# Kernel tuning notes

Measured on AMD Instinct MI355X. Metric: run time of the kernel, lower is better.

## Reference

```python
import jax, jax.numpy as jnp
import numpy as np

KSZ = 5   # local window size per spatial dim
NH = 4    # num_channels -> attention heads
EPS = 1e-6

def rmsnorm(x, w):
    return x * jax.lax.rsqrt(jnp.mean(x * x, axis=-1, keepdims=True) + EPS) * w

def local_windows(x, ksz):
    # x: [B, D, H, W, C] -> [B, D, H, W, ksz**3, C] zero-padded SAME windows
    B, D, H, Wd, C = x.shape
    xt = jnp.transpose(x, (0, 4, 1, 2, 3))  # NCDHW
    p = jax.lax.conv_general_dilated_patches(xt, (ksz, ksz, ksz), (1, 1, 1), 'SAME')
    p = p.reshape(B, C, ksz ** 3, D, H, Wd)  # channel-major patch layout
    return jnp.transpose(p, (0, 3, 4, 5, 2, 1))

def forward(x, norm1_w, attn_norm_w, norm2_w, wq, wk, wv, wo, gate_w, up_w, down_w):
    B, D, H, Wd, C = x.shape
    hd = C // NH
    k3 = KSZ ** 3
    h = rmsnorm(x, norm1_w)
    q = (h @ wq).reshape(B, D, H, Wd, NH, hd)
    k = h @ wk
    v = h @ wv
    kwin = local_windows(k, KSZ).reshape(B, D, H, Wd, k3, NH, hd)
    vwin = local_windows(v, KSZ).reshape(B, D, H, Wd, k3, NH, hd)
    scores = jnp.einsum('bxyzhe,bxyzkhe->bxyzhk', q, kwin) / jnp.sqrt(jnp.float32(hd))
    ones = jnp.ones((1, D, H, Wd, 1), x.dtype)
    valid = local_windows(ones, KSZ)[..., 0] > 0.5  # [1,D,H,W,k3] padding mask
    scores = jnp.where(valid[:, :, :, :, None, :], scores, jnp.float32(-1e9))
    attn = jax.nn.softmax(scores, axis=-1)
    o = jnp.einsum('bxyzhk,bxyzkhe->bxyzhe', attn, vwin).reshape(B, D, H, Wd, C)
    x = x + rmsnorm(o @ wo, attn_norm_w)
    h2 = rmsnorm(x, norm2_w)
    x = x + (jax.nn.silu(h2 @ gate_w) * (h2 @ up_w)) @ down_w  # SwiGLU (dropout=eval)
    return x

def setup_inputs():
    key = jax.random.key(0)
    ks = jax.random.split(key, 8)
    width, hidden = 128, 512
    s = 0.02
    return {
        'x': jax.random.normal(ks[0], (1, 16, 16, 16, width), jnp.float32),
        'norm1_w': jnp.ones((width,), jnp.float32),
        'attn_norm_w': jnp.ones((width,), jnp.float32),
        'norm2_w': jnp.ones((width,), jnp.float32),
        'wq': jax.random.normal(ks[1], (width, width), jnp.float32) * s,
        'wk': jax.random.normal(ks[2], (width, width), jnp.float32) * s,
        'wv': jax.random.normal(ks[3], (width, width), jnp.float32) * s,
        'wo': jax.random.normal(ks[4], (width, width), jnp.float32) * s,
        'gate_w': jax.random.normal(ks[5], (width, hidden), jnp.float32) * s,
        'up_w': jax.random.normal(ks[6], (width, hidden), jnp.float32) * s,
        'down_w': jax.random.normal(ks[7], (hidden, width), jnp.float32) * s,
    }

def reference(x, norm1_w, attn_norm_w, norm2_w, wq, wk, wv, wo, gate_w, up_w, down_w):
    return forward(x, norm1_w, attn_norm_w, norm2_w, wq, wk, wv, wo, gate_w, up_w, down_w)
```

## Files before the change

kernel.cpp:

```cpp
#include <hip/hip_runtime.h>
#include <hip/hip_bf16.h>

#define NVOX 4096
#define C    128
#define HID  512
#define EPSF 1e-6f

typedef __attribute__((ext_vector_type(8))) short bf16x8;
typedef __attribute__((ext_vector_type(4))) float f32x4;

__device__ __forceinline__ short f2bs(float f) {
    __hip_bfloat16 h = __float2bfloat16(f);
    short s; __builtin_memcpy(&s, &h, 2); return s;
}
__device__ __forceinline__ float bs2f(unsigned short u) {
    return __uint_as_float(((unsigned)u) << 16);
}

__device__ __forceinline__ bf16x8 lda(const short* hs, int lane, int ks) {
    int r = lane & 15, g = lane >> 4;
    int col = (ks * 32 + g * 8) ^ ((r & 7) << 3);
    return *(const bf16x8*)(hs + r * 128 + col);
}

__device__ __forceinline__ float wave_rsum(float s) {
    s += __shfl_xor(s, 32); s += __shfl_xor(s, 16); s += __shfl_xor(s, 8);
    s += __shfl_xor(s, 4);  s += __shfl_xor(s, 2);  s += __shfl_xor(s, 1);
    return s;
}

__global__ __launch_bounds__(512) void k_prep(
    const float* __restrict__ wq, const float* __restrict__ wk,
    const float* __restrict__ wv, const float* __restrict__ wo,
    const float* __restrict__ gw, const float* __restrict__ uw,
    const float* __restrict__ dw, short* __restrict__ wsw)
{
    int id = blockIdx.x * 512 + threadIdx.x;
    const float* src; int base, ct, ks, lane, N, KS;
    if (id < 8192) {
        int m = id >> 11, loc = id & 2047;
        src = (m == 0) ? wq : (m == 1) ? wk : (m == 2) ? wv : wo;
        base = m << 14; N = 128; KS = 4;
        ct = loc >> 8; ks = (loc >> 6) & 3; lane = loc & 63;
    } else if (id < 16384) {
        int loc = id - 8192;
        src = gw; base = 65536; N = 512; KS = 4;
        ct = loc >> 8; ks = (loc >> 6) & 3; lane = loc & 63;
    } else if (id < 24576) {
        int loc = id - 16384;
        src = uw; base = 131072; N = 512; KS = 4;
        ct = loc >> 8; ks = (loc >> 6) & 3; lane = loc & 63;
    } else {
        int loc = id - 24576;
        src = dw; base = 196608; N = 128; KS = 16;
        ct = loc >> 10; ks = (loc >> 6) & 15; lane = loc & 63;
    }
    int k0 = ks * 32 + (lane >> 4) * 8;
    int c  = ct * 16 + (lane & 15);
    bf16x8 v;
    #pragma unroll
    for (int j = 0; j < 8; j++) v[j] = f2bs(src[(size_t)(k0 + j) * N + c]);
    *(bf16x8*)(wsw + base + (((ct * KS + ks) * 64 + lane) << 3)) = v;
}

__global__ __launch_bounds__(256) void k_qkv(
    const float* __restrict__ x, const float* __restrict__ n1,
    const short* __restrict__ wsw,
    short* __restrict__ qbf, short* __restrict__ kbf, short* __restrict__ vbf)
{
    __shared__ short hs[2048];
    const int r0 = blockIdx.x * 16, t = threadIdx.x;
    const int w = t >> 6, lane = t & 63;

    #pragma unroll
    for (int i = 0; i < 4; i++) {
        int r = w * 4 + i;
        const float* xp = x + (size_t)(r0 + r) * 128;
        float v0 = xp[lane], v1 = xp[lane + 64];
        float s = wave_rsum(fmaf(v0, v0, v1 * v1));
        float sc = rsqrtf(s * (1.0f / 128.0f) + EPSF);
        int p3 = (r & 7) << 3;
        hs[r * 128 + (lane ^ p3)]        = f2bs(v0 * sc * n1[lane]);
        hs[r * 128 + ((lane + 64) ^ p3)] = f2bs(v1 * sc * n1[lane + 64]);
    }
    __syncthreads();

    bf16x8 af[4];
    #pragma unroll
    for (int ks = 0; ks < 4; ks++) af[ks] = lda(hs, lane, ks);

    const int rb = (lane >> 4) * 4, cl = lane & 15, cb = w * 32;
    #pragma unroll
    for (int m = 0; m < 3; m++) {
        const short* wb = wsw + (m << 14);
        f32x4 a0 = {0.f,0.f,0.f,0.f}, a1 = {0.f,0.f,0.f,0.f};
        #pragma unroll
        for (int ks = 0; ks < 4; ks++) {
            bf16x8 b0 = *(const bf16x8*)(wb + ((((w * 2) * 4 + ks) * 64 + lane) << 3));
            bf16x8 b1 = *(const bf16x8*)(wb + ((((w * 2 + 1) * 4 + ks) * 64 + lane) << 3));
            a0 = __builtin_amdgcn_mfma_f32_16x16x32_bf16(af[ks], b0, a0, 0, 0, 0);
            a1 = __builtin_amdgcn_mfma_f32_16x16x32_bf16(af[ks], b1, a1, 0, 0, 0);
        }
        short* outp = (m == 0) ? qbf : (m == 1) ? kbf : vbf;
        #pragma unroll
        for (int i = 0; i < 4; i++) {
            outp[(size_t)(r0 + rb + i) * 128 + cb + cl]      = f2bs(a0[i]);
            outp[(size_t)(r0 + rb + i) * 128 + cb + 16 + cl] = f2bs(a1[i]);
        }
    }
}

__global__ __launch_bounds__(256) void k_attn(
    const short* __restrict__ qbf, const short* __restrict__ kbf,
    const short* __restrict__ vbf, short* __restrict__ obf)
{
    __shared__ __align__(16) char smem[64128];
    short* K_lds = (short*)smem;
    short* PA    = (short*)smem;
    short* S_lds = (short*)(smem + 30720);
    short* VB    = (short*)(smem + 30720);
    short* Q_lds = (short*)(smem + 61440);
    float* inv   = (float*)(smem + 64000);

    const int b = blockIdx.x, head = blockIdx.y, t = threadIdx.x;
    const int ow = (b & 3) * 4, oh = ((b >> 2) & 3) * 4, od = (b >> 4) * 2;
    const int w = t >> 6, lane = t & 63;
    const int g = lane >> 4, r = lane & 15;

    uint4 v0[4] = {}, v1[4] = {};
    {
        int row = t;
        int lw = row & 7, lh = (row >> 3) & 7, ld = row >> 6;
        int gd = od - 2 + ld, gh = oh - 2 + lh, gw_ = ow - 2 + lw;
        int sv = (((unsigned)gd < 16u) && ((unsigned)gh < 16u) && ((unsigned)gw_ < 16u));
        size_t off = ((size_t)(((gd << 4) | gh) << 4 | gw_)) * 128 + head * 32;
        uint4 kc[4];
        #pragma unroll
        for (int c2 = 0; c2 < 4; c2++) {
            kc[c2] = sv ? *(const uint4*)(kbf + off + c2 * 8) : (uint4){0,0,0,0};
            v0[c2] = sv ? *(const uint4*)(vbf + off + c2 * 8) : (uint4){0,0,0,0};
        }
        #pragma unroll
        for (int c2 = 0; c2 < 4; c2++) *(uint4*)&K_lds[row * 40 + c2 * 8] = kc[c2];

        if (t < 128) {
            int row1 = t + 256;
            int lw1 = row1 & 7, lh1 = (row1 >> 3) & 7, ld1 = row1 >> 6;
            int gd1 = od - 2 + ld1, gh1 = oh - 2 + lh1, gw1 = ow - 2 + lw1;
            int sv1 = (((unsigned)gd1 < 16u) && ((unsigned)gh1 < 16u) && ((unsigned)gw1 < 16u));
            size_t off1 = ((size_t)(((gd1 << 4) | gh1) << 4 | gw1)) * 128 + head * 32;
            uint4 kd[4];
            #pragma unroll
            for (int c2 = 0; c2 < 4; c2++) {
                kd[c2] = sv1 ? *(const uint4*)(kbf + off1 + c2 * 8) : (uint4){0,0,0,0};
                v1[c2] = sv1 ? *(const uint4*)(vbf + off1 + c2 * 8) : (uint4){0,0,0,0};
            }
            #pragma unroll
            for (int c2 = 0; c2 < 4; c2++) *(uint4*)&K_lds[row1 * 40 + c2 * 8] = kd[c2];

            int q = t >> 2, c2q = t & 3;
            int gq = ((od + (q >> 4)) << 8) | ((oh + ((q >> 2) & 3)) << 4) | (ow + (q & 3));
            *(uint4*)&Q_lds[q * 40 + c2q * 8] =
                *(const uint4*)(qbf + (size_t)gq * 128 + head * 32 + c2q * 8);
        }
    }
    __syncthreads();

    {
        bf16x8 bq0 = *(const bf16x8*)(Q_lds + r * 40 + g * 8);
        bf16x8 bq1 = *(const bf16x8*)(Q_lds + (16 + r) * 40 + g * 8);
        #pragma unroll
        for (int jj = 0; jj < 6; jj++) {
            int mt = w + jj * 4;
            bf16x8 ak = *(const bf16x8*)(K_lds + (mt * 16 + r) * 40 + g * 8);
            f32x4 a0 = {0.f,0.f,0.f,0.f}, a1 = {0.f,0.f,0.f,0.f};
            a0 = __builtin_amdgcn_mfma_f32_16x16x32_bf16(ak, bq0, a0, 0, 0, 0);
            a1 = __builtin_amdgcn_mfma_f32_16x16x32_bf16(ak, bq1, a1, 0, 0, 0);
            #pragma unroll
            for (int i = 0; i < 4; i++) {
                int key = mt * 16 + g * 4 + i;
                S_lds[key * 40 + r]      = f2bs(a0[i]);
                S_lds[key * 40 + 16 + r] = f2bs(a1[i]);
            }
        }
    }
    __syncthreads();

    {
        const int q = t >> 3, kl = t & 7;
        const int qw_ = q & 3, qh_ = (q >> 2) & 3, qd_ = q >> 4;
        const float isq = 0.17677669529663687f;
        float mx = -1e30f;
        #pragma unroll
        for (int j = 0; j < 48; j++) {
            int k = kl + (j << 3);
            int lw = k & 7, lh = (k >> 3) & 7, ld = k >> 6;
            int ok = ((unsigned)(ld - qd_) <= 4u) & ((unsigned)(lh - qh_) <= 4u)
                   & ((unsigned)(lw - qw_) <= 4u)
                   & ((unsigned)(od - 2 + ld) < 16u) & ((unsigned)(oh - 2 + lh) < 16u)
                   & ((unsigned)(ow - 2 + lw) < 16u);
            float s = bs2f((unsigned short)S_lds[k * 40 + q]) * isq;
            mx = ok ? fmaxf(mx, s) : mx;
        }
        mx = fmaxf(mx, __shfl_xor(mx, 1));
        mx = fmaxf(mx, __shfl_xor(mx, 2));
        mx = fmaxf(mx, __shfl_xor(mx, 4));
        float ssum = 0.f;
        const int pabase = (q >> 4) * 12 * 512 + (q & 15) * 8 + kl;
        #pragma unroll
        for (int j = 0; j < 48; j++) {
            int k = kl + (j << 3);
            int lw = k & 7, lh = (k >> 3) & 7, ld = k >> 6;
            int ok = ((unsigned)(ld - qd_) <= 4u) & ((unsigned)(lh - qh_) <= 4u)
                   & ((unsigned)(lw - qw_) <= 4u)
                   & ((unsigned)(od - 2 + ld) < 16u) & ((unsigned)(oh - 2 + lh) < 16u)
                   & ((unsigned)(ow - 2 + lw) < 16u);
            float s = bs2f((unsigned short)S_lds[k * 40 + q]) * isq;
            float p = ok ? __expf(s - mx) : 0.f;
            ssum += p;
            PA[pabase + (j >> 2) * 512 + (j & 3) * 128] = f2bs(p);
        }
        ssum += __shfl_xor(ssum, 1);
        ssum += __shfl_xor(ssum, 2);
        ssum += __shfl_xor(ssum, 4);
        if (kl == 0) inv[q] = 1.0f / ssum;
    }
    __syncthreads();

    {
        int row = t;
        int ks = row >> 5, g3 = (row >> 3) & 3, j3 = row & 7;
        const unsigned short* u = (const unsigned short*)v0;
        #pragma unroll
        for (int c = 0; c < 32; c++)
            VB[((c >> 4) * 12 + ks) * 512 + g3 * 128 + (c & 15) * 8 + j3] = (short)u[c];
        if (t < 128) {
            int row1 = t + 256;
            int ks1 = row1 >> 5, g31 = (row1 >> 3) & 3, j31 = row1 & 7;
            const unsigned short* u1 = (const unsigned short*)v1;
            #pragma unroll
            for (int c = 0; c < 32; c++)
                VB[((c >> 4) * 12 + ks1) * 512 + g31 * 128 + (c & 15) * 8 + j31] = (short)u1[c];
        }
    }
    __syncthreads();

    {
        const int mt2 = w >> 1, ct = w & 1;
        f32x4 acc = {0.f,0.f,0.f,0.f};
        #pragma unroll
        for (int ks = 0; ks < 12; ks++) {
            bf16x8 pa = *(const bf16x8*)(PA + (((mt2 * 12 + ks) * 64 + lane) << 3));
            bf16x8 vb = *(const bf16x8*)(VB + (((ct * 12 + ks) * 64 + lane) << 3));
            acc = __builtin_amdgcn_mfma_f32_16x16x32_bf16(pa, vb, acc, 0, 0, 0);
        }
        #pragma unroll
        for (int i = 0; i < 4; i++) {
            int q = mt2 * 16 + g * 4 + i;
            int c = ct * 16 + r;
            int gvox = ((od + (q >> 4)) << 8) | ((oh + ((q >> 2) & 3)) << 4) | (ow + (q & 3));
            obf[(size_t)gvox * 128 + head * 32 + c] = f2bs(acc[i] * inv[q]);
        }
    }
}

__global__ __launch_bounds__(256) void k_post(
    const short* __restrict__ obf, const short* __restrict__ wsw,
    const float* __restrict__ anw, const float* __restrict__ x,
    const float* __restrict__ n2w, float* __restrict__ out)
{
    __shared__ float ybuf[16][132];
    __shared__ float xres[16][128];
    __shared__ short hs[2048];
    __shared__ short gu[16 * 512];

    const int r0 = blockIdx.x * 16, t = threadIdx.x;
    const int w = t >> 6, lane = t & 63;
    const int ar = lane & 15, ag_ = lane >> 4;

    {
        const short* wb = wsw + (3 << 14);
        f32x4 a0 = {0.f,0.f,0.f,0.f}, a1 = {0.f,0.f,0.f,0.f};
        #pragma unroll
        for (int ks = 0; ks < 4; ks++) {
            bf16x8 a = *(const bf16x8*)(obf + (size_t)(r0 + ar) * 128 + ks * 32 + ag_ * 8);
            bf16x8 b0 = *(const bf16x8*)(wb + ((((w * 2) * 4 + ks) * 64 + lane) << 3));
            bf16x8 b1 = *(const bf16x8*)(wb + ((((w * 2 + 1) * 4 + ks) * 64 + lane) << 3));
            a0 = __builtin_amdgcn_mfma_f32_16x16x32_bf16(a, b0, a0, 0, 0, 0);
            a1 = __builtin_amdgcn_mfma_f32_16x16x32_bf16(a, b1, a1, 0, 0, 0);
        }
        #pragma unroll
        for (int i = 0; i < 4; i++) {
            ybuf[ag_ * 4 + i][w * 32 + ar]      = a0[i];
            ybuf[ag_ * 4 + i][w * 32 + 16 + ar] = a1[i];
        }
    }
    __syncthreads();

    #pragma unroll
    for (int i = 0; i < 4; i++) {
        int r = w * 4 + i;
        float y0 = ybuf[r][lane], y1 = ybuf[r][lane + 64];
        float s = wave_rsum(fmaf(y0, y0, y1 * y1));
        float sc = rsqrtf(s * (1.0f / 128.0f) + EPSF);
        const float* xp = x + (size_t)(r0 + r) * 128;
        float xr0 = xp[lane]      + y0 * sc * anw[lane];
        float xr1 = xp[lane + 64] + y1 * sc * anw[lane + 64];
        xres[r][lane] = xr0; xres[r][lane + 64] = xr1;
        float s2 = wave_rsum(fmaf(xr0, xr0, xr1 * xr1));
        float sc2 = rsqrtf(s2 * (1.0f / 128.0f) + EPSF);
        int p3 = (r & 7) << 3;
        hs[r * 128 + (lane ^ p3)]        = f2bs(xr0 * sc2 * n2w[lane]);
        hs[r * 128 + ((lane + 64) ^ p3)] = f2bs(xr1 * sc2 * n2w[lane + 64]);
    }
    __syncthreads();

    {
        const short* gwb = wsw + 65536;
        const short* uwb = wsw + 131072;
        bf16x8 af[4];
        #pragma unroll
        for (int ks = 0; ks < 4; ks++) af[ks] = lda(hs, lane, ks);
        f32x4 ag[8], au[8];
        #pragma unroll
        for (int i = 0; i < 8; i++) { ag[i] = (f32x4){0.f,0.f,0.f,0.f}; au[i] = (f32x4){0.f,0.f,0.f,0.f}; }
        #pragma unroll
        for (int ks = 0; ks < 4; ks++) {
            #pragma unroll
            for (int i = 0; i < 8; i++) {
                int ct = w * 8 + i;
                bf16x8 bg = *(const bf16x8*)(gwb + (((ct * 4 + ks) * 64 + lane) << 3));
                bf16x8 bu = *(const bf16x8*)(uwb + (((ct * 4 + ks) * 64 + lane) << 3));
                ag[i] = __builtin_amdgcn_mfma_f32_16x16x32_bf16(af[ks], bg, ag[i], 0, 0, 0);
                au[i] = __builtin_amdgcn_mfma_f32_16x16x32_bf16(af[ks], bu, au[i], 0, 0, 0);
            }
        }
        #pragma unroll
        for (int i = 0; i < 8; i++) {
            int col = (w * 8 + i) * 16 + ar;
            #pragma unroll
            for (int j = 0; j < 4; j++) {
                int row = ag_ * 4 + j;
                float g = ag[i][j], uu = au[i][j];
                float sg = g / (1.0f + __expf(-g));
                gu[row * 512 + (col ^ ((row & 7) << 3))] = f2bs(sg * uu);
            }
        }
    }
    __syncthreads();

    {
        const short* db = wsw + 196608;
        f32x4 a0 = {0.f,0.f,0.f,0.f}, a1 = {0.f,0.f,0.f,0.f};
        #pragma unroll
        for (int ks = 0; ks < 16; ks++) {
            int col = (ks * 32 + ag_ * 8) ^ ((ar & 7) << 3);
            bf16x8 a = *(const bf16x8*)(gu + ar * 512 + col);
            bf16x8 b0 = *(const bf16x8*)(db + ((((w * 2) * 16 + ks) * 64 + lane) << 3));
            bf16x8 b1 = *(const bf16x8*)(db + ((((w * 2 + 1) * 16 + ks) * 64 + lane) << 3));
            a0 = __builtin_amdgcn_mfma_f32_16x16x32_bf16(a, b0, a0, 0, 0, 0);
            a1 = __builtin_amdgcn_mfma_f32_16x16x32_bf16(a, b1, a1, 0, 0, 0);
        }
        #pragma unroll
        for (int i = 0; i < 4; i++) {
            int row = ag_ * 4 + i;
            size_t i0 = (size_t)(r0 + row) * 128 + w * 32 + ar;
            out[i0]      = xres[row][w * 32 + ar]      + a0[i];
            out[i0 + 16] = xres[row][w * 32 + 16 + ar] + a1[i];
        }
    }
}

extern "C" void kernel_launch(void* const* d_in, const int* in_sizes, int n_in,
                              void* d_out, int out_size, void* d_ws, size_t ws_size,
                              hipStream_t stream)
{
    const float* x   = (const float*)d_in[0];
    const float* n1  = (const float*)d_in[1];
    const float* anw = (const float*)d_in[2];
    const float* n2  = (const float*)d_in[3];
    const float* wq  = (const float*)d_in[4];
    const float* wk  = (const float*)d_in[5];
    const float* wv  = (const float*)d_in[6];
    const float* wo  = (const float*)d_in[7];
    const float* gw  = (const float*)d_in[8];
    const float* uw  = (const float*)d_in[9];
    const float* dw  = (const float*)d_in[10];
    float* out = (float*)d_out;

    float* ws = (float*)d_ws;
    short* qbf = (short*)ws;
    short* kbf = (short*)(ws + 262144);
    short* vbf = (short*)(ws + 524288);
    short* obf = (short*)(ws + 786432);
    short* wsw = (short*)(ws + 1048576);

    k_prep<<<64,  512, 0, stream>>>(wq, wk, wv, wo, gw, uw, dw, wsw);
    k_qkv <<<256, 256, 0, stream>>>(x, n1, wsw, qbf, kbf, vbf);
    dim3 ga(128, 4);
    k_attn<<<ga,  256, 0, stream>>>(qbf, kbf, vbf, obf);
    k_post<<<256, 256, 0, stream>>>(obf, wsw, anw, x, n2, out);
}
```

Baseline: 40.22 us.

## Store Q/K/V head-major and rebalance attention tile loads across threads

The QKV projection kernel now writes Q, K and V in a head-major layout [head][voxel][32] instead of voxel-major [voxel][128]. Each attention block then reads a contiguous 64-byte row per voxel for its head, which should improve load coalescing and locality. The extra halo rows are also moved to threads 128-255 while threads 0-127 load Q, so the two groups split the load work instead of one group doing both. Any other consumer of these buffers must agree on the new layout.

```diff
diff --git a/kernel.cpp b/kernel.cpp
--- a/kernel.cpp
+++ b/kernel.cpp
@@ -89,7 +89,7 @@
     #pragma unroll
     for (int ks = 0; ks < 4; ks++) af[ks] = lda(hs, lane, ks);
 
-    const int rb = (lane >> 4) * 4, cl = lane & 15, cb = w * 32;
+    const int rb = (lane >> 4) * 4, cl = lane & 15;
     #pragma unroll
     for (int m = 0; m < 3; m++) {
         const short* wb = wsw + (m << 14);
@@ -102,10 +102,11 @@
             a1 = __builtin_amdgcn_mfma_f32_16x16x32_bf16(af[ks], b1, a1, 0, 0, 0);
         }
         short* outp = (m == 0) ? qbf : (m == 1) ? kbf : vbf;
+        short* hp = outp + (size_t)w * NVOX * 32;
         #pragma unroll
         for (int i = 0; i < 4; i++) {
-            outp[(size_t)(r0 + rb + i) * 128 + cb + cl]      = f2bs(a0[i]);
-            outp[(size_t)(r0 + rb + i) * 128 + cb + 16 + cl] = f2bs(a1[i]);
+            hp[(size_t)(r0 + rb + i) * 32 + cl]      = f2bs(a0[i]);
+            hp[(size_t)(r0 + rb + i) * 32 + 16 + cl] = f2bs(a1[i]);
         }
     }
 }
@@ -126,6 +127,9 @@
     const int ow = (b & 3) * 4, oh = ((b >> 2) & 3) * 4, od = (b >> 4) * 2;
     const int w = t >> 6, lane = t & 63;
     const int g = lane >> 4, r = lane & 15;
+    const short* kh = kbf + (size_t)head * NVOX * 32;
+    const short* vh = vbf + (size_t)head * NVOX * 32;
+    const short* qh = qbf + (size_t)head * NVOX * 32;
 
     uint4 v0[4] = {}, v1[4] = {};
     {
@@ -133,35 +137,34 @@
         int lw = row & 7, lh = (row >> 3) & 7, ld = row >> 6;
         int gd = od - 2 + ld, gh = oh - 2 + lh, gw_ = ow - 2 + lw;
         int sv = (((unsigned)gd < 16u) && ((unsigned)gh < 16u) && ((unsigned)gw_ < 16u));
-        size_t off = ((size_t)(((gd << 4) | gh) << 4 | gw_)) * 128 + head * 32;
+        size_t off = (size_t)((((gd << 4) | gh) << 4) | gw_) * 32;
         uint4 kc[4];
         #pragma unroll
         for (int c2 = 0; c2 < 4; c2++) {
-            kc[c2] = sv ? *(const uint4*)(kbf + off + c2 * 8) : (uint4){0,0,0,0};
-            v0[c2] = sv ? *(const uint4*)(vbf + off + c2 * 8) : (uint4){0,0,0,0};
+            kc[c2] = sv ? *(const uint4*)(kh + off + c2 * 8) : (uint4){0,0,0,0};
+            v0[c2] = sv ? *(const uint4*)(vh + off + c2 * 8) : (uint4){0,0,0,0};
         }
         #pragma unroll
         for (int c2 = 0; c2 < 4; c2++) *(uint4*)&K_lds[row * 40 + c2 * 8] = kc[c2];
 
-        if (t < 128) {
-            int row1 = t + 256;
+        if (t >= 128) {
+            int row1 = t + 128;
             int lw1 = row1 & 7, lh1 = (row1 >> 3) & 7, ld1 = row1 >> 6;
             int gd1 = od - 2 + ld1, gh1 = oh - 2 + lh1, gw1 = ow - 2 + lw1;
             int sv1 = (((unsigned)gd1 < 16u) && ((unsigned)gh1 < 16u) && ((unsigned)gw1 < 16u));
-            size_t off1 = ((size_t)(((gd1 << 4) | gh1) << 4 | gw1)) * 128 + head * 32;
+            size_t off1 = (size_t)((((gd1 << 4) | gh1) << 4) | gw1) * 32;
             uint4 kd[4];
             #pragma unroll
             for (int c2 = 0; c2 < 4; c2++) {
-                kd[c2] = sv1 ? *(const uint4*)(kbf + off1 + c2 * 8) : (uint4){0,0,0,0};
-                v1[c2] = sv1 ? *(const uint4*)(vbf + off1 + c2 * 8) : (uint4){0,0,0,0};
+                kd[c2] = sv1 ? *(const uint4*)(kh + off1 + c2 * 8) : (uint4){0,0,0,0};
+                v1[c2] = sv1 ? *(const uint4*)(vh + off1 + c2 * 8) : (uint4){0,0,0,0};
             }
             #pragma unroll
             for (int c2 = 0; c2 < 4; c2++) *(uint4*)&K_lds[row1 * 40 + c2 * 8] = kd[c2];
-
+        } else {
             int q = t >> 2, c2q = t & 3;
             int gq = ((od + (q >> 4)) << 8) | ((oh + ((q >> 2) & 3)) << 4) | (ow + (q & 3));
-            *(uint4*)&Q_lds[q * 40 + c2q * 8] =
-                *(const uint4*)(qbf + (size_t)gq * 128 + head * 32 + c2q * 8);
+            *(uint4*)&Q_lds[q * 40 + c2q * 8] = *(const uint4*)(qh + (size_t)gq * 32 + c2q * 8);
         }
     }
     __syncthreads();
@@ -234,8 +237,8 @@
         #pragma unroll
         for (int c = 0; c < 32; c++)
             VB[((c >> 4) * 12 + ks) * 512 + g3 * 128 + (c & 15) * 8 + j3] = (short)u[c];
-        if (t < 128) {
-            int row1 = t + 256;
+        if (t >= 128) {
+            int row1 = t + 128;
             int ks1 = row1 >> 5, g31 = (row1 >> 3) & 3, j31 = row1 & 7;
             const unsigned short* u1 = (const unsigned short*)v1;
             #pragma unroll
```

New measurement: 37.50 us. 1.07x faster.
